# Kernel optimization log

Hardware: AMD Instinct MI355X
Metric: run time of the kernel (lower is better)

The kernel has to match this reference:

```python
import jax, jax.numpy as jnp
import numpy as np

ROPE_DIM = 16      # RotaryEmbedding(dim=16)
MAX_FREQ = 256.0   # freqs_for='pixel'
NUM_HEADS = 16


def _axis_freqs(n):
    # pixel mode: base freqs = linspace(1, max_freq/2, dim//2) * pi, pos = linspace(-1, 1, n)
    base = jnp.linspace(1.0, MAX_FREQ / 2.0, ROPE_DIM // 2) * jnp.pi  # (8,)
    pos = jnp.linspace(-1.0, 1.0, n)                                   # (n,)
    f = pos[:, None] * base[None, :]                                   # (n, 8)
    return jnp.repeat(f, 2, axis=-1)                                   # (n, 16) interleaved pairs


def axial_freqs(T, H, W):
    ft = jnp.broadcast_to(_axis_freqs(T)[:, None, None, :], (T, H, W, ROPE_DIM))
    fh = jnp.broadcast_to(_axis_freqs(H)[None, :, None, :], (T, H, W, ROPE_DIM))
    fw = jnp.broadcast_to(_axis_freqs(W)[None, None, :, :], (T, H, W, ROPE_DIM))
    return jnp.concatenate([ft, fh, fw], axis=-1)  # (T, H, W, 48)


def rotate_half(x):
    # interleaved pairs: (..., d*2) -> rotate each (x1, x2) -> (-x2, x1)
    x = x.reshape(*x.shape[:-1], -1, 2)
    x1, x2 = x[..., 0], x[..., 1]
    return jnp.stack([-x2, x1], axis=-1).reshape(*x.shape[:-2], -1)


def apply_rope(freqs, t):
    # freqs: (T, H, W, rot_dim); t: (B, nh, T, H, W, hd); rotate first rot_dim dims
    rd = freqs.shape[-1]
    tm, tr = t[..., :rd], t[..., rd:]
    tm = tm * jnp.cos(freqs) + rotate_half(tm) * jnp.sin(freqs)
    return jnp.concatenate([tm, tr], axis=-1)


def setup_inputs() -> dict:
    key = jax.random.key(0)
    k1, k2, k3, k4 = jax.random.split(key, 4)
    B, N, C = 2, 2048, 1152
    return {
        "x": jax.random.normal(k1, (B, N, C), dtype=jnp.float32),
        "Wqkv": jax.random.normal(k2, (C, 3 * C), dtype=jnp.float32) * 0.02,
        "Wproj": jax.random.normal(k3, (C, C), dtype=jnp.float32) * 0.02,
        "bproj": jax.random.normal(k4, (C,), dtype=jnp.float32) * 0.02,
        "T": 8, "H": 16, "W": 16,
    }


def reference(x, Wqkv, Wproj, bproj, T, H, W):
    B, N, C = x.shape
    nh = NUM_HEADS
    hd = C // nh
    qkv = (x @ Wqkv).reshape(B, N, 3, nh, hd).transpose(2, 0, 3, 1, 4)  # (3, B, nh, N, hd)
    q, k, v = qkv[0], qkv[1], qkv[2]
    # tokens -> video grid
    q = q.reshape(B, nh, T, H, W, hd)
    k = k.reshape(B, nh, T, H, W, hd)
    freqs = axial_freqs(T, H, W)  # (T, H, W, 48)
    q = apply_rope(freqs, q).reshape(B, nh, N, hd)
    k = apply_rope(freqs, k).reshape(B, nh, N, hd)
    # SDPA (no mask, no dropout in eval / kv_cache=None path)
    scale = 1.0 / np.sqrt(hd)
    attn = jax.nn.softmax(jnp.einsum('bhqd,bhkd->bhqk', q, k) * scale, axis=-1)
    o = jnp.einsum('bhqk,bhkd->bhqd', attn, v)  # (B, nh, N, hd)
    o = o.transpose(0, 2, 1, 3).reshape(B, N, C)
    return o @ Wproj + bproj
```

## Files before the change

kernel.cpp:

```cpp
#include <hip/hip_runtime.h>
#include <hip/hip_bf16.h>

#define B_   2
#define N_   2048
#define C_   1152
#define NH   16
#define HD   72
#define HDP  96
#define HDV  80
#define QSTR 3584
#define KROW 104
#define VROW 72
#define KVB  64
#define KCH  832
#define VCH  720
#define TCH  1552
#define WCH  388

typedef __attribute__((ext_vector_type(8))) short bf16x8;
typedef __attribute__((ext_vector_type(4))) float f32x4;

__device__ __forceinline__ short f2bf(float f) {
  union { float fv; unsigned int u; } v; v.fv = f;
  unsigned int r = v.u + 0x7fffu + ((v.u >> 16) & 1u);
  return (short)(r >> 16);
}

__device__ __forceinline__ float bf2f(short s) {
  union { unsigned u; float f; } v; v.u = ((unsigned)(unsigned short)s) << 16;
  return v.f;
}

__device__ __forceinline__ unsigned pack_bf16(float a, float b) {
  union { __hip_bfloat162 h; unsigned u; } c;
  c.h = __float22bfloat162_rn(make_float2(a, b));
  return c.u;
}

__device__ __forceinline__ void gload_lds16(const short* g, short* l) {
  __builtin_amdgcn_global_load_lds(
      (const __attribute__((address_space(1))) unsigned int*)g,
      (__attribute__((address_space(3))) unsigned int*)l, 16, 0, 0);
}

__global__ __launch_bounds__(256) void prep(
    const float* __restrict__ x, short* __restrict__ xb,
    const float* __restrict__ Wqkv, short* __restrict__ Wt,
    const float* __restrict__ Wproj, short* __restrict__ Wpt) {
  int bid = blockIdx.x;
  if (bid < 4608) {
    const int i = bid * 256 + threadIdx.x;
    float4 v = ((const float4*)x)[i];
    short4 s;
    s.x = f2bf(v.x); s.y = f2bf(v.y); s.z = f2bf(v.z); s.w = f2bf(v.w);
    ((short4*)xb)[i] = s;
    return;
  }
  bid -= 4608;
  const float* src; short* dst; int Cc, bx, by;
  if (bid < 4032) {
    bx = bid % 112; by = bid / 112; src = Wqkv; dst = Wt; Cc = 3456;
  } else {
    bid -= 4032;
    bx = bid % 36; by = bid / 36; src = Wproj; dst = Wpt; Cc = 1152;
  }
  __shared__ float tile[32][33];
  const int c0 = bx * 32, r0 = by * 32;
  const int tx = threadIdx.x & 31, ty = threadIdx.x >> 5;
  for (int i = ty; i < 32; i += 8)
    tile[i][tx] = (c0 + tx < Cc) ? src[(long)(r0 + i) * Cc + c0 + tx] : 0.f;
  __syncthreads();
  for (int i = ty; i < 32; i += 8)
    dst[(long)(c0 + i) * 1152 + r0 + tx] = f2bf(tile[tx][i]);
}

template<bool BIAS, bool OBF>
__global__ __launch_bounds__(256, 2) void gemm_bt(
    const short* __restrict__ A, const short* __restrict__ Bt,
    void* __restrict__ Cv, const float* __restrict__ bias,
    int M, int N, int K) {
  __shared__ __align__(16) short As[2][128 * 32];
  __shared__ __align__(16) short Bs[2][128 * 32];
  const int t = threadIdx.x;
  const int lane = t & 63, wid = t >> 6;
  const int fr = lane & 15, fq = lane >> 4;

  int lin = blockIdx.y * gridDim.x + blockIdx.x;
  const int q8 = (int)(gridDim.x * gridDim.y) >> 3;
  lin = (lin & 7) * q8 + (lin >> 3);
  const int bm = lin / (int)gridDim.x;
  const int bn = lin - bm * (int)gridDim.x;

  const int wr = (wid >> 1) * 64, wc = (wid & 1) * 64;

  const int srow = t >> 2;
  const int scol = (t & 3) * 8;
  const short* Ag = A + (long)(bm * 128 + srow) * K + scol;
  const short* Bg = Bt + (long)(bn * 128 + srow) * K + scol;

  f32x4 acc[4][4] = {};

  auto STAGE = [&](int kt, int bufi) {
    gload_lds16(Ag + kt * 32,                &As[bufi][t * 8]);
    gload_lds16(Ag + kt * 32 + (long)64 * K, &As[bufi][2048 + t * 8]);
    gload_lds16(Bg + kt * 32,                &Bs[bufi][t * 8]);
    gload_lds16(Bg + kt * 32 + (long)64 * K, &Bs[bufi][2048 + t * 8]);
  };

  const int NKT = K / 32;
  STAGE(0, 0);

  for (int kt = 0; kt < NKT; ++kt) {
    const int cur = kt & 1;
    if (kt + 1 < NKT) {
      STAGE(kt + 1, cur ^ 1);
      asm volatile("s_waitcnt vmcnt(4)" ::: "memory");
    } else {
      asm volatile("s_waitcnt vmcnt(0)" ::: "memory");
    }
    __builtin_amdgcn_s_barrier();

    bf16x8 af[4], bf[4];
    #pragma unroll
    for (int i = 0; i < 4; ++i)
      af[i] = *(const bf16x8*)(&As[cur][(wr + i * 16 + fr) * 32 + fq * 8]);
    #pragma unroll
    for (int j = 0; j < 4; ++j)
      bf[j] = *(const bf16x8*)(&Bs[cur][(wc + j * 16 + fr) * 32 + fq * 8]);
    __builtin_amdgcn_s_setprio(1);
    #pragma unroll
    for (int i = 0; i < 4; ++i)
      #pragma unroll
      for (int j = 0; j < 4; ++j)
        acc[i][j] = __builtin_amdgcn_mfma_f32_16x16x32_bf16(af[i], bf[j], acc[i][j], 0, 0, 0);
    __builtin_amdgcn_s_setprio(0);
    __builtin_amdgcn_s_barrier();
  }

  #pragma unroll
  for (int i = 0; i < 4; ++i) {
    #pragma unroll
    for (int j = 0; j < 4; ++j) {
      const long row0 = (long)bm * 128 + wr + i * 16 + fq * 4;
      const int col = bn * 128 + wc + j * 16 + fr;
      const float bv = BIAS ? bias[col] : 0.f;
      #pragma unroll
      for (int r = 0; r < 4; ++r) {
        const float val = acc[i][j][r] + bv;
        if constexpr (OBF)
          ((short*)Cv)[(row0 + r) * (long)N + col] = f2bf(val);
        else
          ((float*)Cv)[(row0 + r) * (long)N + col] = val;
      }
    }
  }
}

__global__ __launch_bounds__(512, 2) void gemm_bt256(
    const short* __restrict__ A, const short* __restrict__ Bt,
    short* __restrict__ Cv, int M, int N, int K) {
  __shared__ __align__(16) short As[2][256 * 64];
  __shared__ __align__(16) short Bs[2][256 * 64];
  const int t = threadIdx.x;
  const int lane = t & 63, wid = t >> 6;
  const int fr = lane & 15, fq = lane >> 4;
  const int wm = wid >> 2, wn = wid & 3;
  const int rx = fr & 7;

  int lin = blockIdx.y * gridDim.x + blockIdx.x;
  const int q8 = (int)(gridDim.x * gridDim.y) >> 3;
  lin = (lin & 7) * q8 + (lin >> 3);
  const int bm = lin / (int)gridDim.x;
  const int bn = lin - bm * (int)gridDim.x;

  int soff[4];
  #pragma unroll
  for (int r = 0; r < 4; ++r) {
    const int p = r * 512 + t;
    const int row = p >> 3, pc = p & 7;
    soff[r] = row * K + (pc ^ (row & 7)) * 8;
  }
  const short* Ag = A + (long)bm * 256 * K;
  const short* Bg = Bt + (long)bn * 256 * K;

  f32x4 acc[8][4] = {};

  const int NKT = K / 64;
  #pragma unroll
  for (int r = 0; r < 4; ++r)
    gload_lds16(Ag + soff[r], &As[0][(r * 512 + t) * 8]);
  #pragma unroll
  for (int r = 0; r < 4; ++r)
    gload_lds16(Bg + soff[r], &Bs[0][(r * 512 + t) * 8]);

  for (int kt = 0; kt < NKT; ++kt) {
    const int cur = kt & 1;
    const bool pre = (kt + 1 < NKT);
    asm volatile("s_waitcnt vmcnt(0)" ::: "memory");
    __builtin_amdgcn_s_barrier();
    const short* Ac = &As[cur][0];
    const short* Bc = &Bs[cur][0];
    bf16x8 af[4][2], bf0[2][2], bf1[2][2];

    if (pre) {
      #pragma unroll
      for (int r = 0; r < 4; ++r)
        gload_lds16(Ag + soff[r] + (kt + 1) * 64, &As[cur ^ 1][(r * 512 + t) * 8]);
    }
    #pragma unroll
    for (int i = 0; i < 4; ++i)
      #pragma unroll
      for (int kk = 0; kk < 2; ++kk)
        af[i][kk] = *(const bf16x8*)(Ac + (wm * 128 + i * 16 + fr) * 64 + (((kk * 4 + fq) ^ rx) * 8));
    #pragma unroll
    for (int j = 0; j < 2; ++j)
      #pragma unroll
      for (int kk = 0; kk < 2; ++kk)
        bf0[j][kk] = *(const bf16x8*)(Bc + (wn * 64 + j * 16 + fr) * 64 + (((kk * 4 + fq) ^ rx) * 8));
    __builtin_amdgcn_s_setprio(1);
    #pragma unroll
    for (int i = 0; i < 4; ++i)
      #pragma unroll
      for (int j = 0; j < 2; ++j)
        #pragma unroll
        for (int kk = 0; kk < 2; ++kk)
          acc[i][j] = __builtin_amdgcn_mfma_f32_16x16x32_bf16(af[i][kk], bf0[j][kk], acc[i][j], 0, 0, 0);
    __builtin_amdgcn_s_setprio(0);

    if (pre) {
      #pragma unroll
      for (int r = 0; r < 4; ++r)
        gload_lds16(Bg + soff[r] + (kt + 1) * 64, &Bs[cur ^ 1][(r * 512 + t) * 8]);
    }
    #pragma unroll
    for (int j = 0; j < 2; ++j)
      #pragma unroll
      for (int kk = 0; kk < 2; ++kk)
        bf1[j][kk] = *(const bf16x8*)(Bc + (wn * 64 + 32 + j * 16 + fr) * 64 + (((kk * 4 + fq) ^ rx) * 8));
    __builtin_amdgcn_s_setprio(1);
    #pragma unroll
    for (int i = 0; i < 4; ++i)
      #pragma unroll
      for (int j = 0; j < 2; ++j)
        #pragma unroll
        for (int kk = 0; kk < 2; ++kk)
          acc[i][2 + j] = __builtin_amdgcn_mfma_f32_16x16x32_bf16(af[i][kk], bf1[j][kk], acc[i][2 + j], 0, 0, 0);
    __builtin_amdgcn_s_setprio(0);

    #pragma unroll
    for (int i = 0; i < 4; ++i)
      #pragma unroll
      for (int kk = 0; kk < 2; ++kk)
        af[i][kk] = *(const bf16x8*)(Ac + (wm * 128 + 64 + i * 16 + fr) * 64 + (((kk * 4 + fq) ^ rx) * 8));
    __builtin_amdgcn_s_setprio(1);
    #pragma unroll
    for (int i = 0; i < 4; ++i)
      #pragma unroll
      for (int j = 0; j < 2; ++j)
        #pragma unroll
        for (int kk = 0; kk < 2; ++kk)
          acc[4 + i][j] = __builtin_amdgcn_mfma_f32_16x16x32_bf16(af[i][kk], bf0[j][kk], acc[4 + i][j], 0, 0, 0);
    __builtin_amdgcn_s_setprio(0);

    __builtin_amdgcn_s_setprio(1);
    #pragma unroll
    for (int i = 0; i < 4; ++i)
      #pragma unroll
      for (int j = 0; j < 2; ++j)
        #pragma unroll
        for (int kk = 0; kk < 2; ++kk)
          acc[4 + i][2 + j] = __builtin_amdgcn_mfma_f32_16x16x32_bf16(af[i][kk], bf1[j][kk], acc[4 + i][2 + j], 0, 0, 0);
    __builtin_amdgcn_s_setprio(0);
  }

  #pragma unroll
  for (int mi = 0; mi < 8; ++mi) {
    #pragma unroll
    for (int j = 0; j < 4; ++j) {
      const long row0 = (long)bm * 256 + wm * 128 + (mi >> 2) * 64 + (mi & 3) * 16 + fq * 4;
      const int col = bn * 256 + wn * 64 + j * 16 + fr;
      #pragma unroll
      for (int r = 0; r < 4; ++r)
        Cv[(row0 + r) * (long)N + col] = f2bf(acc[mi][j][r]);
    }
  }
}

__global__ __launch_bounds__(256) void rope_pack(
    const short* __restrict__ QKV, short* __restrict__ Qp,
    short* __restrict__ Kp, short* __restrict__ Vt) {
  const int blk = blockIdx.x;
  const int nt = blk & 15;
  const int h = (blk >> 4) & 15;
  const int b = blk >> 8;
  const int t = threadIdx.x;
  const int n0 = nt * 128;
  const float qscale = 0.17002324f;
  const float PI = 3.14159265358979323846f;

  for (int which = 0; which < 2; ++which) {
    short* dst = which ? Kp : Qp;
    const float sc = which ? 1.0f : qscale;
    for (int idx = t; idx < 128 * 48; idx += 256) {
      const int r = idx / 48;
      const int p = idx - r * 48;
      const int n = n0 + r;
      float vx = 0.f, vy = 0.f;
      if (p < 36) {
        short2 v2 = *(const short2*)(QKV + ((long)(b * N_ + n)) * QSTR + which * C_ + h * HD + 2 * p);
        vx = bf2f(v2.x); vy = bf2f(v2.y);
      }
      float o0 = vx, o1 = vy;
      if (p < 24) {
        float pos;
        if (p < 8)       pos = -1.f + (2.f / 7.f)  * (float)(n >> 8);
        else if (p < 16) pos = -1.f + (2.f / 15.f) * (float)((n >> 4) & 15);
        else             pos = -1.f + (2.f / 15.f) * (float)(n & 15);
        const float base = (1.f + (127.f / 7.f) * (float)(p & 7)) * PI;
        const float f = pos * base;
        const float cs = cosf(f), sn = sinf(f);
        o0 = vx * cs - vy * sn;
        o1 = vy * cs + vx * sn;
      }
      short2 ov; ov.x = f2bf(o0 * sc); ov.y = f2bf(o1 * sc);
      *(short2*)(dst + (((long)(b * NH + h)) * N_ + n) * HDP + 2 * p) = ov;
    }
  }

  __shared__ short vt[128][82];
  for (int idx = t; idx < 128 * 40; idx += 256) {
    const int r = idx / 40, p = idx - r * 40;
    short2 v2; v2.x = 0; v2.y = 0;
    if (p < 36)
      v2 = *(const short2*)(QKV + ((long)(b * N_ + n0 + r)) * QSTR + 2 * C_ + h * HD + 2 * p);
    *(short2*)(&vt[r][2 * p]) = v2;
  }
  __syncthreads();
  for (int idx = t; idx < HDV * 128; idx += 256) {
    const int d = idx >> 7, nn = idx & 127;
    const int c = nn & 31;
    const int nsrc = (nn & 96) | (((c >> 2) & 1) * 16 + ((c >> 3) & 3) * 4 + (c & 3));
    Vt[(((long)(b * NH + h)) * HDV + d) * N_ + n0 + nn] = vt[nsrc][d];
  }
}

__global__ __launch_bounds__(256, 2) void attn(
    const short* __restrict__ Qp, const short* __restrict__ Kp,
    const short* __restrict__ Vt, short* __restrict__ Aproj) {
  __shared__ __align__(16) short KV[3][TCH * 8];
  int blk = blockIdx.x;
  blk = (blk & 7) * 64 + (blk >> 3);
  const int qt = blk & 15;
  const int h = (blk >> 4) & 15;
  const int b = blk >> 8;
  const int t = threadIdx.x, lane = t & 63, wid = t >> 6;
  const int fr = lane & 15, fq = lane >> 4;

  const long bh = (long)(b * NH + h);
  const short* Qg = Qp + (bh * N_ + qt * 128) * HDP;
  const short* Kg = Kp + bh * N_ * HDP;
  const short* Vg = Vt + bh * HDV * N_;

  const short* sb[7];
  int sstr[7];
  #pragma unroll
  for (int it = 0; it < 7; ++it) {
    int g = wid * WCH + (it < 6 ? it * 64 + lane : 384 + lane);
    if (g >= TCH) g = TCH - 1;
    if (g < KCH) {
      const int r = g / 13, c = g - r * 13;
      sb[it] = Kg + r * HDP + (c < 12 ? c * 8 : 0);
      sstr[it] = KVB * HDP;
    } else {
      const int v = g - KCH;
      const int r = v / 9, c = v - r * 9;
      sb[it] = Vg + r * N_ + (c < 8 ? c * 8 : 0);
      sstr[it] = KVB;
    }
  }

  bf16x8 qf[2][3];
  #pragma unroll
  for (int i = 0; i < 2; ++i)
    #pragma unroll
    for (int kk = 0; kk < 3; ++kk)
      qf[i][kk] = *(const bf16x8*)(Qg + (wid * 32 + i * 16 + fr) * HDP + kk * 32 + fq * 8);

  f32x4 accO[2][5] = {};
  float l_[2] = {0.f, 0.f};

  auto STAGE = [&](int kt, int bufi) {
    short* D = &KV[bufi][0];
    #pragma unroll
    for (int it = 0; it < 6; ++it)
      gload_lds16(sb[it] + kt * sstr[it], D + (wid * WCH + it * 64 + lane) * 8);
    if (lane < 4)
      gload_lds16(sb[6] + kt * sstr[6], D + (wid * WCH + 384 + lane) * 8);
  };

  STAGE(0, 0);
  STAGE(1, 1);

  for (int kt = 0; kt < 32; ++kt) {
    if (kt < 31) asm volatile("s_waitcnt vmcnt(7)" ::: "memory");
    else         asm volatile("s_waitcnt vmcnt(0)" ::: "memory");
    __builtin_amdgcn_s_barrier();
    if (kt < 30) STAGE(kt + 2, (kt + 2) % 3);

    const short* KsC = &KV[kt % 3][0];
    const short* VsC = KsC + KCH * 8;

    f32x4 s[2][4] = {};
    __builtin_amdgcn_s_setprio(1);
    #pragma unroll
    for (int j = 0; j < 4; ++j) {
      #pragma unroll
      for (int kk = 0; kk < 3; ++kk) {
        bf16x8 kf = *(const bf16x8*)(KsC + (j * 16 + fr) * KROW + (kk * 4 + fq) * 8);
        s[0][j] = __builtin_amdgcn_mfma_f32_16x16x32_bf16(kf, qf[0][kk], s[0][j], 0, 0, 0);
        s[1][j] = __builtin_amdgcn_mfma_f32_16x16x32_bf16(kf, qf[1][kk], s[1][j], 0, 0, 0);
      }
    }
    __builtin_amdgcn_s_setprio(0);

    #pragma unroll
    for (int i = 0; i < 2; ++i) {
      float psum = 0.f;
      #pragma unroll
      for (int j = 0; j < 4; ++j)
        #pragma unroll
        for (int r = 0; r < 4; ++r) {
          const float p = __builtin_amdgcn_exp2f(s[i][j][r]);
          s[i][j][r] = p;
          psum += p;
        }
      l_[i] += psum;
    }

    __builtin_amdgcn_s_setprio(1);
    #pragma unroll
    for (int g = 0; g < 2; ++g) {
      union { unsigned u[4]; bf16x8 v; } pf0, pf1;
      pf0.u[0] = pack_bf16(s[0][2 * g][0],     s[0][2 * g][1]);
      pf0.u[1] = pack_bf16(s[0][2 * g][2],     s[0][2 * g][3]);
      pf0.u[2] = pack_bf16(s[0][2 * g + 1][0], s[0][2 * g + 1][1]);
      pf0.u[3] = pack_bf16(s[0][2 * g + 1][2], s[0][2 * g + 1][3]);
      pf1.u[0] = pack_bf16(s[1][2 * g][0],     s[1][2 * g][1]);
      pf1.u[1] = pack_bf16(s[1][2 * g][2],     s[1][2 * g][3]);
      pf1.u[2] = pack_bf16(s[1][2 * g + 1][0], s[1][2 * g + 1][1]);
      pf1.u[3] = pack_bf16(s[1][2 * g + 1][2], s[1][2 * g + 1][3]);
      #pragma unroll
      for (int jd = 0; jd < 5; ++jd) {
        bf16x8 vf = *(const bf16x8*)(VsC + (jd * 16 + fr) * VROW + (g * 4 + fq) * 8);
        accO[0][jd] = __builtin_amdgcn_mfma_f32_16x16x32_bf16(pf0.v, vf, accO[0][jd], 0, 0, 0);
        accO[1][jd] = __builtin_amdgcn_mfma_f32_16x16x32_bf16(pf1.v, vf, accO[1][jd], 0, 0, 0);
      }
    }
    __builtin_amdgcn_s_setprio(0);
  }

  #pragma unroll
  for (int i = 0; i < 2; ++i) {
    l_[i] += __shfl_xor(l_[i], 16);
    l_[i] += __shfl_xor(l_[i], 32);
  }
  float linv[2] = {1.f / l_[0], 1.f / l_[1]};
  #pragma unroll
  for (int i = 0; i < 2; ++i) {
    float li[4];
    #pragma unroll
    for (int r = 0; r < 4; ++r) li[r] = __shfl(linv[i], fq * 4 + r);
    #pragma unroll
    for (int r = 0; r < 4; ++r) {
      const long n = qt * 128 + wid * 32 + i * 16 + fq * 4 + r;
      #pragma unroll
      for (int jd = 0; jd < 5; ++jd) {
        const int d = jd * 16 + fr;
        if (d < HD)
          Aproj[((long)b * N_ + n) * C_ + h * HD + d] = f2bf(accO[i][jd][r] * li[r]);
      }
    }
  }
}

extern "C" void kernel_launch(void* const* d_in, const int* in_sizes, int n_in,
                              void* d_out, int out_size, void* d_ws, size_t ws_size,
                              hipStream_t stream) {
  const float* x     = (const float*)d_in[0];
  const float* Wqkv  = (const float*)d_in[1];
  const float* Wproj = (const float*)d_in[2];
  const float* bproj = (const float*)d_in[3];
  float* out = (float*)d_out;

  char* ws = (char*)d_ws;
  short* QKVb = (short*)ws;         size_t off = (size_t)4096 * QSTR * 2;
  short* xb  = (short*)(ws + off);  off += (size_t)4096 * 1152 * 2;
  short* Wt  = (short*)(ws + off);  off += (size_t)QSTR * 1152 * 2;
  short* Wpt = (short*)(ws + off);  off += (size_t)1152 * 1152 * 2;
  short* Qp  = (short*)(ws + off);  off += (size_t)B_ * NH * N_ * HDP * 2;
  short* Kp  = (short*)(ws + off);  off += (size_t)B_ * NH * N_ * HDP * 2;
  short* Vt  = (short*)(ws + off);  off += (size_t)B_ * NH * HDV * N_ * 2;
  short* Ap  = (short*)(ws + off);  off += (size_t)4096 * 1152 * 2;

  prep<<<4608 + 4032 + 1296, 256, 0, stream>>>(x, xb, Wqkv, Wt, Wproj, Wpt);
  gemm_bt256<<<dim3(QSTR / 256, 4096 / 256), 512, 0, stream>>>(
      xb, Wt, QKVb, 4096, QSTR, 1152);
  rope_pack<<<B_ * NH * (N_ / 128), 256, 0, stream>>>(QKVb, Qp, Kp, Vt);
  attn<<<B_ * NH * (N_ / 128), 256, 0, stream>>>(Qp, Kp, Vt, Ap);
  gemm_bt<true, false><<<dim3(1152 / 128, 4096 / 128), 256, 0, stream>>>(
      Ap, Wpt, (void*)out, bproj, 4096, 1152, 1152);
}
```

Baseline: 179.1 us.

## Load V fragments directly from global into registers instead of staging in LDS

```diff
diff --git a/kernel.cpp b/kernel.cpp
--- a/kernel.cpp
+++ b/kernel.cpp
@@ -10,12 +10,8 @@
 #define HDV  80
 #define QSTR 3584
 #define KROW 104
-#define VROW 72
 #define KVB  64
 #define KCH  832
-#define VCH  720
-#define TCH  1552
-#define WCH  388
 
 typedef __attribute__((ext_vector_type(8))) short bf16x8;
 typedef __attribute__((ext_vector_type(4))) float f32x4;
@@ -347,7 +343,7 @@
 __global__ __launch_bounds__(256, 2) void attn(
     const short* __restrict__ Qp, const short* __restrict__ Kp,
     const short* __restrict__ Vt, short* __restrict__ Aproj) {
-  __shared__ __align__(16) short KV[3][TCH * 8];
+  __shared__ __align__(16) short Ks[3][KCH * 8];
   int blk = blockIdx.x;
   blk = (blk & 7) * 64 + (blk >> 3);
   const int qt = blk & 15;
@@ -361,22 +357,12 @@
   const short* Kg = Kp + bh * N_ * HDP;
   const short* Vg = Vt + bh * HDV * N_;
 
-  const short* sb[7];
-  int sstr[7];
-  #pragma unroll
-  for (int it = 0; it < 7; ++it) {
-    int g = wid * WCH + (it < 6 ? it * 64 + lane : 384 + lane);
-    if (g >= TCH) g = TCH - 1;
-    if (g < KCH) {
-      const int r = g / 13, c = g - r * 13;
-      sb[it] = Kg + r * HDP + (c < 12 ? c * 8 : 0);
-      sstr[it] = KVB * HDP;
-    } else {
-      const int v = g - KCH;
-      const int r = v / 9, c = v - r * 9;
-      sb[it] = Vg + r * N_ + (c < 8 ? c * 8 : 0);
-      sstr[it] = KVB;
-    }
+  const short* sb[4];
+  #pragma unroll
+  for (int it = 0; it < 4; ++it) {
+    const int g = wid * 208 + (it < 3 ? it * 64 + lane : 192 + (lane & 15));
+    const int r = g / 13, c = g - r * 13;
+    sb[it] = Kg + r * HDP + (c < 12 ? c * 8 : 0);
   }
 
   bf16x8 qf[2][3];
@@ -390,25 +376,32 @@
   float l_[2] = {0.f, 0.f};
 
   auto STAGE = [&](int kt, int bufi) {
-    short* D = &KV[bufi][0];
-    #pragma unroll
-    for (int it = 0; it < 6; ++it)
-      gload_lds16(sb[it] + kt * sstr[it], D + (wid * WCH + it * 64 + lane) * 8);
-    if (lane < 4)
-      gload_lds16(sb[6] + kt * sstr[6], D + (wid * WCH + 384 + lane) * 8);
+    short* D = &Ks[bufi][0];
+    #pragma unroll
+    for (int it = 0; it < 3; ++it)
+      gload_lds16(sb[it] + kt * (KVB * HDP), D + (wid * 208 + it * 64 + lane) * 8);
+    if (lane < 16)
+      gload_lds16(sb[3] + kt * (KVB * HDP), D + (wid * 208 + 192 + lane) * 8);
   };
 
   STAGE(0, 0);
   STAGE(1, 1);
 
   for (int kt = 0; kt < 32; ++kt) {
-    if (kt < 31) asm volatile("s_waitcnt vmcnt(7)" ::: "memory");
+    if (kt < 31) asm volatile("s_waitcnt vmcnt(4)" ::: "memory");
     else         asm volatile("s_waitcnt vmcnt(0)" ::: "memory");
     __builtin_amdgcn_s_barrier();
+
+    bf16x8 vf[2][5];
+    #pragma unroll
+    for (int g = 0; g < 2; ++g)
+      #pragma unroll
+      for (int jd = 0; jd < 5; ++jd)
+        vf[g][jd] = *(const bf16x8*)(Vg + (long)(jd * 16 + fr) * N_ + kt * KVB + (g * 4 + fq) * 8);
+
     if (kt < 30) STAGE(kt + 2, (kt + 2) % 3);
 
-    const short* KsC = &KV[kt % 3][0];
-    const short* VsC = KsC + KCH * 8;
+    const short* KsC = &Ks[kt % 3][0];
 
     f32x4 s[2][4] = {};
     __builtin_amdgcn_s_setprio(1);
@@ -451,9 +444,8 @@
       pf1.u[3] = pack_bf16(s[1][2 * g + 1][2], s[1][2 * g + 1][3]);
       #pragma unroll
       for (int jd = 0; jd < 5; ++jd) {
-        bf16x8 vf = *(const bf16x8*)(VsC + (jd * 16 + fr) * VROW + (g * 4 + fq) * 8);
-        accO[0][jd] = __builtin_amdgcn_mfma_f32_16x16x32_bf16(pf0.v, vf, accO[0][jd], 0, 0, 0);
-        accO[1][jd] = __builtin_amdgcn_mfma_f32_16x16x32_bf16(pf1.v, vf, accO[1][jd], 0, 0, 0);
+        accO[0][jd] = __builtin_amdgcn_mfma_f32_16x16x32_bf16(pf0.v, vf[g][jd], accO[0][jd], 0, 0, 0);
+        accO[1][jd] = __builtin_amdgcn_mfma_f32_16x16x32_bf16(pf1.v, vf[g][jd], accO[1][jd], 0, 0, 0);
       }
     }
     __builtin_amdgcn_s_setprio(0);
```

Measured after the change: 210.7 us. 1.18x slower.

## Software-pipeline QK^T of next tile with softmax and PV of current tile

Applied to the files above, without the earlier changes.

```diff
diff --git a/kernel.cpp b/kernel.cpp
--- a/kernel.cpp
+++ b/kernel.cpp
@@ -13,7 +13,6 @@
 #define VROW 72
 #define KVB  64
 #define KCH  832
-#define VCH  720
 #define TCH  1552
 #define WCH  388
 
@@ -297,33 +296,44 @@
   const int n0 = nt * 128;
   const float qscale = 0.17002324f;
   const float PI = 3.14159265358979323846f;
-
-  for (int which = 0; which < 2; ++which) {
-    short* dst = which ? Kp : Qp;
-    const float sc = which ? 1.0f : qscale;
-    for (int idx = t; idx < 128 * 48; idx += 256) {
-      const int r = idx / 48;
-      const int p = idx - r * 48;
-      const int n = n0 + r;
+  const long bhn = ((long)(b * NH + h)) * N_;
+
+  for (int idx = t; idx < 128 * 48; idx += 256) {
+    const int r = idx / 48;
+    const int p = idx - r * 48;
+    const int n = n0 + r;
+    float cs = 1.f, sn = 0.f;
+    if (p < 24) {
+      float pos;
+      if (p < 8)       pos = -1.f + (2.f / 7.f)  * (float)(n >> 8);
+      else if (p < 16) pos = -1.f + (2.f / 15.f) * (float)((n >> 4) & 15);
+      else             pos = -1.f + (2.f / 15.f) * (float)(n & 15);
+      const float base = (1.f + (127.f / 7.f) * (float)(p & 7)) * PI;
+      const float f = pos * base;
+      cs = cosf(f); sn = sinf(f);
+    }
+    const long rowbase = ((long)(b * N_ + n)) * QSTR + h * HD + 2 * p;
+    {
       float vx = 0.f, vy = 0.f;
       if (p < 36) {
-        short2 v2 = *(const short2*)(QKV + ((long)(b * N_ + n)) * QSTR + which * C_ + h * HD + 2 * p);
+        short2 v2 = *(const short2*)(QKV + rowbase);
         vx = bf2f(v2.x); vy = bf2f(v2.y);
       }
-      float o0 = vx, o1 = vy;
-      if (p < 24) {
-        float pos;
-        if (p < 8)       pos = -1.f + (2.f / 7.f)  * (float)(n >> 8);
-        else if (p < 16) pos = -1.f + (2.f / 15.f) * (float)((n >> 4) & 15);
-        else             pos = -1.f + (2.f / 15.f) * (float)(n & 15);
-        const float base = (1.f + (127.f / 7.f) * (float)(p & 7)) * PI;
-        const float f = pos * base;
-        const float cs = cosf(f), sn = sinf(f);
-        o0 = vx * cs - vy * sn;
-        o1 = vy * cs + vx * sn;
+      const float o0 = vx * cs - vy * sn;
+      const float o1 = vy * cs + vx * sn;
+      short2 ov; ov.x = f2bf(o0 * qscale); ov.y = f2bf(o1 * qscale);
+      *(short2*)(Qp + (bhn + n) * HDP + 2 * p) = ov;
+    }
+    {
+      float vx = 0.f, vy = 0.f;
+      if (p < 36) {
+        short2 v2 = *(const short2*)(QKV + rowbase + C_);
+        vx = bf2f(v2.x); vy = bf2f(v2.y);
       }
-      short2 ov; ov.x = f2bf(o0 * sc); ov.y = f2bf(o1 * sc);
-      *(short2*)(dst + (((long)(b * NH + h)) * N_ + n) * HDP + 2 * p) = ov;
+      const float o0 = vx * cs - vy * sn;
+      const float o1 = vy * cs + vx * sn;
+      short2 ov; ov.x = f2bf(o0); ov.y = f2bf(o1);
+      *(short2*)(Kp + (bhn + n) * HDP + 2 * p) = ov;
     }
   }
 
@@ -343,6 +353,74 @@
     Vt[(((long)(b * NH + h)) * HDV + d) * N_ + n0 + nn] = vt[nsrc][d];
   }
 }
+
+#define QKT_STEP(BUFI, S)                                                      \
+  {                                                                            \
+    const short* KsC_ = &KV[(BUFI)][0];                                        \
+    __builtin_amdgcn_s_setprio(1);                                             \
+    _Pragma("unroll")                                                          \
+    for (int j = 0; j < 4; ++j) {                                              \
+      _Pragma("unroll")                                                        \
+      for (int kk = 0; kk < 3; ++kk) {                                         \
+        bf16x8 kf = *(const bf16x8*)(KsC_ + (j * 16 + fr) * KROW + (kk * 4 + fq) * 8); \
+        S[0][j] = __builtin_amdgcn_mfma_f32_16x16x32_bf16(kf, qf[0][kk], S[0][j], 0, 0, 0); \
+        S[1][j] = __builtin_amdgcn_mfma_f32_16x16x32_bf16(kf, qf[1][kk], S[1][j], 0, 0, 0); \
+      }                                                                        \
+    }                                                                          \
+    __builtin_amdgcn_s_setprio(0);                                             \
+  }
+
+#define ATTN_STEP(T, SCUR, SNEXT)                                              \
+  {                                                                            \
+    const int t_ = (T);                                                        \
+          \
+    _Pragma("unroll")                                                          \
+    for (int i = 0; i < 2; ++i) {                                              \
+      float psum = 0.f;                                                        \
+      _Pragma("unroll")                                                        \
+      for (int j = 0; j < 4; ++j)                                              \
+        _Pragma("unroll")                                                      \
+        for (int r = 0; r < 4; ++r) {                                          \
+          const float p = __builtin_amdgcn_exp2f(SCUR[i][j][r]);               \
+          SCUR[i][j][r] = p;                                                   \
+          psum += p;                                                           \
+        }                                                                      \
+      l_[i] += psum;                                                           \
+    }                                                                          \
+    asm volatile("s_waitcnt vmcnt(0)" ::: "memory");                           \
+    __builtin_amdgcn_s_barrier();                                              \
+    if (t_ + 2 < 32) STAGE(t_ + 2, (t_ + 2) % 3);                              \
+    if (t_ + 1 < 32) {                                                         \
+      _Pragma("unroll")                                                        \
+      for (int i = 0; i < 2; ++i)                                              \
+        _Pragma("unroll")                                                      \
+        for (int j = 0; j < 4; ++j)                                            \
+          SNEXT[i][j] = (f32x4){0.f, 0.f, 0.f, 0.f};                           \
+      QKT_STEP((t_ + 1) % 3, SNEXT);                                           \
+    }                                                                          \
+                    \
+    const short* VsC_ = &KV[t_ % 3][KCH * 8];                                  \
+    __builtin_amdgcn_s_setprio(1);                                             \
+    _Pragma("unroll")                                                          \
+    for (int g = 0; g < 2; ++g) {                                              \
+      union { unsigned u[4]; bf16x8 v; } pf0, pf1;                             \
+      pf0.u[0] = pack_bf16(SCUR[0][2 * g][0],     SCUR[0][2 * g][1]);          \
+      pf0.u[1] = pack_bf16(SCUR[0][2 * g][2],     SCUR[0][2 * g][3]);          \
+      pf0.u[2] = pack_bf16(SCUR[0][2 * g + 1][0], SCUR[0][2 * g + 1][1]);      \
+      pf0.u[3] = pack_bf16(SCUR[0][2 * g + 1][2], SCUR[0][2 * g + 1][3]);      \
+      pf1.u[0] = pack_bf16(SCUR[1][2 * g][0],     SCUR[1][2 * g][1]);          \
+      pf1.u[1] = pack_bf16(SCUR[1][2 * g][2],     SCUR[1][2 * g][3]);          \
+      pf1.u[2] = pack_bf16(SCUR[1][2 * g + 1][0], SCUR[1][2 * g + 1][1]);      \
+      pf1.u[3] = pack_bf16(SCUR[1][2 * g + 1][2], SCUR[1][2 * g + 1][3]);      \
+      _Pragma("unroll")                                                        \
+      for (int jd = 0; jd < 5; ++jd) {                                         \
+        bf16x8 vf = *(const bf16x8*)(VsC_ + (jd * 16 + fr) * VROW + (g * 4 + fq) * 8); \
+        accO[0][jd] = __builtin_amdgcn_mfma_f32_16x16x32_bf16(pf0.v, vf, accO[0][jd], 0, 0, 0); \
+        accO[1][jd] = __builtin_amdgcn_mfma_f32_16x16x32_bf16(pf1.v, vf, accO[1][jd], 0, 0, 0); \
+      }                                                                        \
+    }                                                                          \
+    __builtin_amdgcn_s_setprio(0);                                             \
+  }
 
 __global__ __launch_bounds__(256, 2) void attn(
     const short* __restrict__ Qp, const short* __restrict__ Kp,
@@ -400,63 +478,20 @@
 
   STAGE(0, 0);
   STAGE(1, 1);
-
-  for (int kt = 0; kt < 32; ++kt) {
-    if (kt < 31) asm volatile("s_waitcnt vmcnt(7)" ::: "memory");
-    else         asm volatile("s_waitcnt vmcnt(0)" ::: "memory");
-    __builtin_amdgcn_s_barrier();
-    if (kt < 30) STAGE(kt + 2, (kt + 2) % 3);
-
-    const short* KsC = &KV[kt % 3][0];
-    const short* VsC = KsC + KCH * 8;
-
-    f32x4 s[2][4] = {};
-    __builtin_amdgcn_s_setprio(1);
-    #pragma unroll
-    for (int j = 0; j < 4; ++j) {
-      #pragma unroll
-      for (int kk = 0; kk < 3; ++kk) {
-        bf16x8 kf = *(const bf16x8*)(KsC + (j * 16 + fr) * KROW + (kk * 4 + fq) * 8);
-        s[0][j] = __builtin_amdgcn_mfma_f32_16x16x32_bf16(kf, qf[0][kk], s[0][j], 0, 0, 0);
-        s[1][j] = __builtin_amdgcn_mfma_f32_16x16x32_bf16(kf, qf[1][kk], s[1][j], 0, 0, 0);
-      }
-    }
-    __builtin_amdgcn_s_setprio(0);
-
-    #pragma unroll
-    for (int i = 0; i < 2; ++i) {
-      float psum = 0.f;
-      #pragma unroll
-      for (int j = 0; j < 4; ++j)
-        #pragma unroll
-        for (int r = 0; r < 4; ++r) {
-          const float p = __builtin_amdgcn_exp2f(s[i][j][r]);
-          s[i][j][r] = p;
-          psum += p;
-        }
-      l_[i] += psum;
-    }
-
-    __builtin_amdgcn_s_setprio(1);
-    #pragma unroll
-    for (int g = 0; g < 2; ++g) {
-      union { unsigned u[4]; bf16x8 v; } pf0, pf1;
-      pf0.u[0] = pack_bf16(s[0][2 * g][0],     s[0][2 * g][1]);
-      pf0.u[1] = pack_bf16(s[0][2 * g][2],     s[0][2 * g][3]);
-      pf0.u[2] = pack_bf16(s[0][2 * g + 1][0], s[0][2 * g + 1][1]);
-      pf0.u[3] = pack_bf16(s[0][2 * g + 1][2], s[0][2 * g + 1][3]);
-      pf1.u[0] = pack_bf16(s[1][2 * g][0],     s[1][2 * g][1]);
-      pf1.u[1] = pack_bf16(s[1][2 * g][2],     s[1][2 * g][3]);
-      pf1.u[2] = pack_bf16(s[1][2 * g + 1][0], s[1][2 * g + 1][1]);
-      pf1.u[3] = pack_bf16(s[1][2 * g + 1][2], s[1][2 * g + 1][3]);
-      #pragma unroll
-      for (int jd = 0; jd < 5; ++jd) {
-        bf16x8 vf = *(const bf16x8*)(VsC + (jd * 16 + fr) * VROW + (g * 4 + fq) * 8);
-        accO[0][jd] = __builtin_amdgcn_mfma_f32_16x16x32_bf16(pf0.v, vf, accO[0][jd], 0, 0, 0);
-        accO[1][jd] = __builtin_amdgcn_mfma_f32_16x16x32_bf16(pf1.v, vf, accO[1][jd], 0, 0, 0);
-      }
-    }
-    __builtin_amdgcn_s_setprio(0);
+  asm volatile("s_waitcnt vmcnt(7)" ::: "memory");
+  __builtin_amdgcn_s_barrier();
+
+  f32x4 sA[2][4], sB[2][4];
+  #pragma unroll
+  for (int i = 0; i < 2; ++i)
+    #pragma unroll
+    for (int j = 0; j < 4; ++j)
+      sA[i][j] = (f32x4){0.f, 0.f, 0.f, 0.f};
+  QKT_STEP(0, sA);
+
+  for (int kt2 = 0; kt2 < 16; ++kt2) {
+    ATTN_STEP(2 * kt2,     sA, sB);
+    ATTN_STEP(2 * kt2 + 1, sB, sA);
   }
 
   #pragma unroll
```

After: 172.0 us. -4.0%, faster.
